# Optimization experiments

Hardware: AMD Instinct MI355X
Metric: run time of the kernel (lower is better)

The kernel has to match this reference:

```python
import jax, jax.numpy as jnp
import numpy as np

B, SQ, SKV, D = 4, 4096, 4096, 64

def setup_inputs() -> dict:
    key = jax.random.key(0)
    kq, kk, kv = jax.random.split(key, 3)
    return {
        "q": jax.random.normal(kq, (B, SQ, D), dtype=jnp.float32),
        "k": jax.random.normal(kk, (B, SKV, D), dtype=jnp.float32),
        "v": jax.random.normal(kv, (B, SKV, D), dtype=jnp.float32),
        "inv_scale_factor": 8,
        "is_training": 0,
    }

def reference(q, k, v, inv_scale_factor, is_training):
    # qk = q @ k^T, divided by inv_scale_factor, softmax over keys
    scores = jnp.einsum("bqd,bkd->bqk", q, k) / inv_scale_factor  # [B,SQ,SKV]
    attn = jax.nn.softmax(scores, axis=-1)
    # dropout is deterministic identity (eval mode, is_training=0)
    out = jnp.einsum("bqk,bkd->bqd", attn, v)  # [B,SQ,D]
    # should_apply_residual before loop
    out = out + q
    # 3-iteration chain: residual add + normalization add (+2q), dropout (identity),
    # sigmoid, clamp(0,1)
    for _ in range(3):
        out = out + 2.0 * q
        out = jax.nn.sigmoid(out)
        out = jnp.clip(out, 0.0, 1.0)
    return out
```

## Files before the change

### kernel.cpp

```cpp
#include <hip/hip_runtime.h>

#define SQd 4096
#define SKVd 4096
#define DDIM 64
#define BK 32
#define NG 8
#define NTILES (SKVd / BK)
#define TPG (NTILES / NG)
#define TILE_BYTES 2048
#define KWS_BYTES (4 * NTILES * TILE_BYTES)
#define BROWS 32

typedef float floatx4 __attribute__((ext_vector_type(4)));

__device__ inline long long mk64(int lo, int hi) {
    int2 t; t.x = lo; t.y = hi;
    return __builtin_bit_cast(long long, t);
}
template <bool HI>
__device__ inline int pk2(float a, float b, int old) {
    return __builtin_amdgcn_cvt_pk_fp8_f32(a, b, old, HI);
}

struct CombS {
    float Ored[BROWS][4][68];
    float Lred[BROWS][NG];
};

__global__ __launch_bounds__(256)
void prepack_kernel(const float* __restrict__ k, const float* __restrict__ v,
                    char* __restrict__ ws)
{
    __shared__ __align__(16) float Kt[BK][68];
    __shared__ __align__(16) float Vt[BK][68];

    const int blk  = blockIdx.x;
    const int b    = blk >> 7;
    const int tile = blk & (NTILES - 1);
    const int tid  = threadIdx.x;

    const size_t base = ((size_t)b * SKVd + tile * BK) * DDIM;
    {
        const int row = tid >> 3, col = (tid & 7) * 8;
        const float4 k0 = *(const float4*)(k + base + (size_t)row * DDIM + col);
        const float4 k1 = *(const float4*)(k + base + (size_t)row * DDIM + col + 4);
        *(float4*)&Kt[row][col] = k0; *(float4*)&Kt[row][col + 4] = k1;
        const float4 v0 = *(const float4*)(v + base + (size_t)row * DDIM + col);
        const float4 v1 = *(const float4*)(v + base + (size_t)row * DDIM + col + 4);
        *(float4*)&Vt[row][col] = v0; *(float4*)&Vt[row][col + 4] = v1;
    }
    __syncthreads();

    const int lane = tid & 63;
    const int l16  = lane & 15;
    const int quad = lane >> 4;
    const int f    = tid >> 6;

    int w[4];
    size_t off;
    if (f < 2) {
        const float* s0 = &Kt[f * 16 + l16][quad * 8];
        const float* s1 = &Kt[f * 16 + l16][32 + quad * 8];
        w[0] = pk2<false>(s0[0], s0[1], 0); w[0] = pk2<true>(s0[2], s0[3], w[0]);
        w[1] = pk2<false>(s0[4], s0[5], 0); w[1] = pk2<true>(s0[6], s0[7], w[1]);
        w[2] = pk2<false>(s1[0], s1[1], 0); w[2] = pk2<true>(s1[2], s1[3], w[2]);
        w[3] = pk2<false>(s1[4], s1[5], 0); w[3] = pk2<true>(s1[6], s1[7], w[3]);
        off = ((size_t)(b * NTILES + tile) * 2 + f) * 1024 + lane * 16;
    } else {
        const int p = f - 2;
        float vv[16];
        #pragma unroll
        for (int j2 = 0; j2 < 16; ++j2) {
            const int nb = 2 * p + (j2 >> 3);
            const int j  = j2 & 7;
            vv[j2] = Vt[16 * (j >> 2) + quad * 4 + (j & 3)][nb * 16 + l16];
        }
        #pragma unroll
        for (int i = 0; i < 4; ++i) {
            w[i] = pk2<false>(vv[4 * i], vv[4 * i + 1], 0);
            w[i] = pk2<true>(vv[4 * i + 2], vv[4 * i + 3], w[i]);
        }
        off = (size_t)KWS_BYTES + ((size_t)(b * NTILES + tile) * 2 + p) * 1024 + lane * 16;
    }
    int4 o4; o4.x = w[0]; o4.y = w[1]; o4.z = w[2]; o4.w = w[3];
    *(int4*)(ws + off) = o4;
}

__global__ __launch_bounds__(512, 4)
void fattn_kernel(const float* __restrict__ q, const int* __restrict__ isf_p,
                  const char* __restrict__ kws, const char* __restrict__ vws,
                  float* __restrict__ out)
{
    __shared__ __align__(16) CombS C;

    const int tid  = threadIdx.x;
    const int g    = tid >> 6;
    const int lane = tid & 63;
    const int l16  = lane & 15;
    const int quad = lane >> 4;

    const int bidx  = blockIdx.x;
    const int b     = bidx >> 7;
    const int qbase = (bidx & 127) * BROWS;

    const float scale = 1.44269504088896340736f / (float)(*isf_p);
    const float SINIT = -4.0f * 1.44269504088896340736f;

    long long qf[2][2];
    #pragma unroll
    for (int qg = 0; qg < 2; ++qg) {
        const int qrow = qbase + qg * 16 + l16;
        const float* qp = q + ((size_t)b * SQd + qrow) * DDIM + quad * 8;
        #pragma unroll
        for (int dh = 0; dh < 2; ++dh) {
            const float4 a0 = *(const float4*)(qp + dh * 32);
            const float4 a1 = *(const float4*)(qp + dh * 32 + 4);
            int lo = pk2<false>(a0.x * scale, a0.y * scale, 0);
            lo     = pk2<true>(a0.z * scale, a0.w * scale, lo);
            int hi = pk2<false>(a1.x * scale, a1.y * scale, 0);
            hi     = pk2<true>(a1.z * scale, a1.w * scale, hi);
            qf[qg][dh] = mk64(lo, hi);
        }
    }

    const char* kg = kws + (size_t)(b * NTILES + g * TPG) * TILE_BYTES + lane * 16;
    const char* vg = vws + (size_t)(b * NTILES + g * TPG) * TILE_BYTES + lane * 16;
    const int phase = bidx & (TPG - 1);

    floatx4 o[2][4];
    float l_acc[2];
    #pragma unroll
    for (int qg = 0; qg < 2; ++qg) {
        l_acc[qg] = 0.0f;
        #pragma unroll
        for (int nb = 0; nb < 4; ++nb)
            #pragma unroll
            for (int r = 0; r < 4; ++r) o[qg][nb][r] = 0.0f;
    }
    const floatx4 sinit = {SINIT, SINIT, SINIT, SINIT};

    auto load = [&](int4* kd, int4* vd, int t) {
        const size_t off = (size_t)((t + phase) & (TPG - 1)) * TILE_BYTES;
        kd[0] = *(const int4*)(kg + off);
        kd[1] = *(const int4*)(kg + off + 1024);
        vd[0] = *(const int4*)(vg + off);
        vd[1] = *(const int4*)(vg + off + 1024);
    };
    auto compute = [&](const int4* kc, const int4* vc) {
        const long long k00 = mk64(kc[0].x, kc[0].y), k01 = mk64(kc[0].z, kc[0].w);
        const long long k10 = mk64(kc[1].x, kc[1].y), k11 = mk64(kc[1].z, kc[1].w);
        const long long v0 = mk64(vc[0].x, vc[0].y), v1 = mk64(vc[0].z, vc[0].w);
        const long long v2 = mk64(vc[1].x, vc[1].y), v3 = mk64(vc[1].z, vc[1].w);
        #pragma unroll
        for (int qg = 0; qg < 2; ++qg) {
            floatx4 s0 = sinit, s1 = sinit;
            s0 = __builtin_amdgcn_mfma_f32_16x16x32_fp8_fp8(k00, qf[qg][0], s0, 0, 0, 0);
            s0 = __builtin_amdgcn_mfma_f32_16x16x32_fp8_fp8(k01, qf[qg][1], s0, 0, 0, 0);
            s1 = __builtin_amdgcn_mfma_f32_16x16x32_fp8_fp8(k10, qf[qg][0], s1, 0, 0, 0);
            s1 = __builtin_amdgcn_mfma_f32_16x16x32_fp8_fp8(k11, qf[qg][1], s1, 0, 0, 0);
            const float p00 = __builtin_amdgcn_exp2f(s0[0]);
            const float p01 = __builtin_amdgcn_exp2f(s0[1]);
            const float p02 = __builtin_amdgcn_exp2f(s0[2]);
            const float p03 = __builtin_amdgcn_exp2f(s0[3]);
            const float p10 = __builtin_amdgcn_exp2f(s1[0]);
            const float p11 = __builtin_amdgcn_exp2f(s1[1]);
            const float p12 = __builtin_amdgcn_exp2f(s1[2]);
            const float p13 = __builtin_amdgcn_exp2f(s1[3]);
            l_acc[qg] += (p00 + p01) + (p02 + p03) + (p10 + p11) + (p12 + p13);
            int lo = pk2<false>(p00, p01, 0); lo = pk2<true>(p02, p03, lo);
            int hi = pk2<false>(p10, p11, 0); hi = pk2<true>(p12, p13, hi);
            const long long pf = mk64(lo, hi);
            o[qg][0] = __builtin_amdgcn_mfma_f32_16x16x32_fp8_fp8(pf, v0, o[qg][0], 0, 0, 0);
            o[qg][1] = __builtin_amdgcn_mfma_f32_16x16x32_fp8_fp8(pf, v1, o[qg][1], 0, 0, 0);
            o[qg][2] = __builtin_amdgcn_mfma_f32_16x16x32_fp8_fp8(pf, v2, o[qg][2], 0, 0, 0);
            o[qg][3] = __builtin_amdgcn_mfma_f32_16x16x32_fp8_fp8(pf, v3, o[qg][3], 0, 0, 0);
        }
    };

    int4 kb0[2], vb0[2], kb1[2], vb1[2];
    load(kb0, vb0, 0);
    #pragma unroll
    for (int t = 0; t < TPG / 2; ++t) {
        load(kb1, vb1, 2 * t + 1);
        compute(kb0, vb0);
        load(kb0, vb0, (2 * t + 2) & (TPG - 1));
        compute(kb1, vb1);
    }

    #pragma unroll
    for (int qg = 0; qg < 2; ++qg) {
        l_acc[qg] += __shfl_xor(l_acc[qg], 16);
        l_acc[qg] += __shfl_xor(l_acc[qg], 32);
    }
    if (quad == 0) {
        #pragma unroll
        for (int qg = 0; qg < 2; ++qg)
            C.Lred[qg * 16 + l16][g] = l_acc[qg];
    }

    if (g < 4) {
        #pragma unroll
        for (int qg = 0; qg < 2; ++qg)
            #pragma unroll
            for (int nb = 0; nb < 4; ++nb)
                #pragma unroll
                for (int r = 0; r < 4; ++r)
                    C.Ored[qg * 16 + quad * 4 + r][g][nb * 16 + l16] = o[qg][nb][r];
    }
    __syncthreads();
    if (g >= 4) {
        #pragma unroll
        for (int qg = 0; qg < 2; ++qg)
            #pragma unroll
            for (int nb = 0; nb < 4; ++nb)
                #pragma unroll
                for (int r = 0; r < 4; ++r)
                    C.Ored[qg * 16 + quad * 4 + r][g - 4][nb * 16 + l16] += o[qg][nb][r];
    }
    __syncthreads();

    {
        const int row = tid >> 4;
        const int d4  = (tid & 15) * 4;
        float l = 0.0f;
        #pragma unroll
        for (int gg = 0; gg < NG; ++gg) l += C.Lred[row][gg];
        const float rl = 1.0f / l;
        float xs[4] = {0.f, 0.f, 0.f, 0.f};
        #pragma unroll
        for (int s = 0; s < 4; ++s) {
            const float4 t4 = *(const float4*)&C.Ored[row][s][d4];
            xs[0] += t4.x; xs[1] += t4.y; xs[2] += t4.z; xs[3] += t4.w;
        }
        const size_t idx = ((size_t)b * SQd + qbase + row) * DDIM + d4;
        const float4 q4 = *(const float4*)(q + idx);
        const float qs[4] = {q4.x, q4.y, q4.z, q4.w};
        #pragma unroll
        for (int c = 0; c < 4; ++c) {
            float x = xs[c] * rl + qs[c];
            #pragma unroll
            for (int itc = 0; itc < 3; ++itc) {
                x = x + 2.0f * qs[c];
                x = 1.0f / (1.0f + __expf(-x));
                x = fminf(fmaxf(x, 0.0f), 1.0f);
            }
            xs[c] = x;
        }
        const float4 r4 = {xs[0], xs[1], xs[2], xs[3]};
        *(float4*)(out + idx) = r4;
    }
}

extern "C" void kernel_launch(void* const* d_in, const int* in_sizes, int n_in,
                              void* d_out, int out_size, void* d_ws, size_t ws_size,
                              hipStream_t stream) {
    const float* q = (const float*)d_in[0];
    const float* k = (const float*)d_in[1];
    const float* v = (const float*)d_in[2];
    const int* isf = (const int*)d_in[3];
    float* out = (float*)d_out;
    char* ws = (char*)d_ws;

    prepack_kernel<<<dim3(4 * NTILES), dim3(256), 0, stream>>>(k, v, ws);

    const int nblocks = 4 * (SQd / BROWS);
    fattn_kernel<<<dim3(nblocks), dim3(512), 0, stream>>>(
        q, isf, ws, ws + KWS_BYTES, out);
}
```

Measured before the change: 88.14 us.

## Switch attention MFMAs to 32x32x64 scaled FP8 with repacked K/V layout

Replaces the 16x16x32 FP8 MFMA sequence with the gfx950 32x32x64 scaled f8f6f4 MFMA for both QK^T and PV, processing 64-key chunks per iteration. The prepack kernel writes K and V in a new fragment layout to match the larger MFMA operands, and the loop now loads the next chunk's K and V separately, each after the MFMAs that consume the current one. This is meant to cut MFMA instruction count and issue overhead and to give fewer, wider loads. In exchange it raises per-thread register pressure (16-wide accumulators and score vectors) and depends on the new layout being correct.

```diff
diff --git a/kernel.cpp b/kernel.cpp
--- a/kernel.cpp
+++ b/kernel.cpp
@@ -6,20 +6,26 @@
 #define BK 32
 #define NG 8
 #define NTILES (SKVd / BK)
+#define NCHUNK (NTILES / 2)
 #define TPG (NTILES / NG)
-#define TILE_BYTES 2048
-#define KWS_BYTES (4 * NTILES * TILE_BYTES)
+#define CPG (TPG / 2)
+#define KWS_BYTES ((size_t)4 * NTILES * 2048)
 #define BROWS 32
 
-typedef float floatx4 __attribute__((ext_vector_type(4)));
-
-__device__ inline long long mk64(int lo, int hi) {
-    int2 t; t.x = lo; t.y = hi;
-    return __builtin_bit_cast(long long, t);
-}
+typedef float floatx4  __attribute__((ext_vector_type(4)));
+typedef float floatx16 __attribute__((ext_vector_type(16)));
+typedef int   intx8    __attribute__((ext_vector_type(8)));
+
 template <bool HI>
 __device__ inline int pk2(float a, float b, int old) {
     return __builtin_amdgcn_cvt_pk_fp8_f32(a, b, old, HI);
+}
+
+__device__ inline intx8 mk8(int4 a, int4 b) {
+    intx8 r;
+    r[0] = a.x; r[1] = a.y; r[2] = a.z; r[3] = a.w;
+    r[4] = b.x; r[5] = b.y; r[6] = b.z; r[7] = b.w;
+    return r;
 }
 
 struct CombS {
@@ -52,38 +58,35 @@
     __syncthreads();
 
     const int lane = tid & 63;
-    const int l16  = lane & 15;
-    const int quad = lane >> 4;
-    const int f    = tid >> 6;
-
-    int w[4];
-    size_t off;
-    if (f < 2) {
-        const float* s0 = &Kt[f * 16 + l16][quad * 8];
-        const float* s1 = &Kt[f * 16 + l16][32 + quad * 8];
-        w[0] = pk2<false>(s0[0], s0[1], 0); w[0] = pk2<true>(s0[2], s0[3], w[0]);
-        w[1] = pk2<false>(s0[4], s0[5], 0); w[1] = pk2<true>(s0[6], s0[7], w[1]);
-        w[2] = pk2<false>(s1[0], s1[1], 0); w[2] = pk2<true>(s1[2], s1[3], w[2]);
-        w[3] = pk2<false>(s1[4], s1[5], 0); w[3] = pk2<true>(s1[6], s1[7], w[3]);
-        off = ((size_t)(b * NTILES + tile) * 2 + f) * 1024 + lane * 16;
-    } else {
-        const int p = f - 2;
-        float vv[16];
-        #pragma unroll
-        for (int j2 = 0; j2 < 16; ++j2) {
-            const int nb = 2 * p + (j2 >> 3);
-            const int j  = j2 & 7;
-            vv[j2] = Vt[16 * (j >> 2) + quad * 4 + (j & 3)][nb * 16 + l16];
-        }
-        #pragma unroll
-        for (int i = 0; i < 4; ++i) {
-            w[i] = pk2<false>(vv[4 * i], vv[4 * i + 1], 0);
-            w[i] = pk2<true>(vv[4 * i + 2], vv[4 * i + 3], w[i]);
-        }
-        off = (size_t)KWS_BYTES + ((size_t)(b * NTILES + tile) * 2 + p) * 1024 + lane * 16;
-    }
-    int4 o4; o4.x = w[0]; o4.y = w[1]; o4.z = w[2]; o4.w = w[3];
-    *(int4*)(ws + off) = o4;
+    const int q4   = tid >> 6;
+    const int l31  = lane & 31;
+    const int u    = lane >> 5;
+
+    {
+        const float* s = &Kt[l31][u * 32 + q4 * 8];
+        int w0 = pk2<false>(s[0], s[1], 0); w0 = pk2<true>(s[2], s[3], w0);
+        int w1 = pk2<false>(s[4], s[5], 0); w1 = pk2<true>(s[6], s[7], w1);
+        int2 o2; o2.x = w0; o2.y = w1;
+        *(int2*)(ws + (size_t)(b * NTILES + tile) * 2048 + lane * 32 + q4 * 8) = o2;
+    }
+    {
+        const int h  = q4 >> 1;
+        const int rh = (q4 & 1) * 8;
+        float p[8];
+        #pragma unroll
+        for (int i = 0; i < 8; ++i) {
+            const int r   = rh + i;
+            const int key = (r & 3) + 8 * (r >> 2) + 4 * u;
+            p[i] = Vt[key][h * 32 + l31];
+        }
+        int w0 = pk2<false>(p[0], p[1], 0); w0 = pk2<true>(p[2], p[3], w0);
+        int w1 = pk2<false>(p[4], p[5], 0); w1 = pk2<true>(p[6], p[7], w1);
+        int2 o2; o2.x = w0; o2.y = w1;
+        const size_t voff = KWS_BYTES
+            + ((size_t)(b * NCHUNK + (tile >> 1)) * 2 + h) * 2048
+            + lane * 32 + (tile & 1) * 16 + rh;
+        *(int2*)(ws + voff) = o2;
+    }
 }
 
 __global__ __launch_bounds__(512, 4)
@@ -91,13 +94,13 @@
                   const char* __restrict__ kws, const char* __restrict__ vws,
                   float* __restrict__ out)
 {
-    __shared__ __align__(16) CombS C;
+    __shared__ CombS C;
 
     const int tid  = threadIdx.x;
     const int g    = tid >> 6;
     const int lane = tid & 63;
-    const int l16  = lane & 15;
-    const int quad = lane >> 4;
+    const int l31  = lane & 31;
+    const int u    = lane >> 5;
 
     const int bidx  = blockIdx.x;
     const int b     = bidx >> 7;
@@ -106,116 +109,97 @@
     const float scale = 1.44269504088896340736f / (float)(*isf_p);
     const float SINIT = -4.0f * 1.44269504088896340736f;
 
-    long long qf[2][2];
+    intx8 qf;
+    {
+        const float* qp = q + ((size_t)b * SQd + qbase + l31) * DDIM + u * 32;
+        #pragma unroll
+        for (int d = 0; d < 8; ++d) {
+            const float4 a = *(const float4*)(qp + 4 * d);
+            int w = pk2<false>(a.x * scale, a.y * scale, 0);
+            w     = pk2<true >(a.z * scale, a.w * scale, w);
+            qf[d] = w;
+        }
+    }
+
+    const char* kg = kws + (size_t)(b * NTILES + g * TPG) * 2048 + lane * 32;
+    const char* vg = vws + (size_t)(b * NCHUNK + g * CPG) * 4096 + lane * 32;
+    const int cph  = bidx & (CPG - 1);
+
+    floatx16 sinit16, o0, o1;
     #pragma unroll
-    for (int qg = 0; qg < 2; ++qg) {
-        const int qrow = qbase + qg * 16 + l16;
-        const float* qp = q + ((size_t)b * SQd + qrow) * DDIM + quad * 8;
-        #pragma unroll
-        for (int dh = 0; dh < 2; ++dh) {
-            const float4 a0 = *(const float4*)(qp + dh * 32);
-            const float4 a1 = *(const float4*)(qp + dh * 32 + 4);
-            int lo = pk2<false>(a0.x * scale, a0.y * scale, 0);
-            lo     = pk2<true>(a0.z * scale, a0.w * scale, lo);
-            int hi = pk2<false>(a1.x * scale, a1.y * scale, 0);
-            hi     = pk2<true>(a1.z * scale, a1.w * scale, hi);
-            qf[qg][dh] = mk64(lo, hi);
-        }
-    }
-
-    const char* kg = kws + (size_t)(b * NTILES + g * TPG) * TILE_BYTES + lane * 16;
-    const char* vg = vws + (size_t)(b * NTILES + g * TPG) * TILE_BYTES + lane * 16;
-    const int phase = bidx & (TPG - 1);
-
-    floatx4 o[2][4];
-    float l_acc[2];
+    for (int i = 0; i < 16; ++i) { sinit16[i] = SINIT; o0[i] = 0.f; o1[i] = 0.f; }
+    float l_acc = 0.f;
+
+    int4 kA0, kA1, kB0, kB1, vA0, vA1, vB0, vB1;
+    auto loadK = [&](int c) {
+        const size_t off = (size_t)((c + cph) & (CPG - 1)) * 4096;
+        kA0 = *(const int4*)(kg + off);        kA1 = *(const int4*)(kg + off + 16);
+        kB0 = *(const int4*)(kg + off + 2048); kB1 = *(const int4*)(kg + off + 2064);
+    };
+    auto loadV = [&](int c) {
+        const size_t off = (size_t)((c + cph) & (CPG - 1)) * 4096;
+        vA0 = *(const int4*)(vg + off);        vA1 = *(const int4*)(vg + off + 16);
+        vB0 = *(const int4*)(vg + off + 2048); vB1 = *(const int4*)(vg + off + 2064);
+    };
+
+    loadK(0); loadV(0);
     #pragma unroll
-    for (int qg = 0; qg < 2; ++qg) {
-        l_acc[qg] = 0.0f;
-        #pragma unroll
-        for (int nb = 0; nb < 4; ++nb)
-            #pragma unroll
-            for (int r = 0; r < 4; ++r) o[qg][nb][r] = 0.0f;
-    }
-    const floatx4 sinit = {SINIT, SINIT, SINIT, SINIT};
-
-    auto load = [&](int4* kd, int4* vd, int t) {
-        const size_t off = (size_t)((t + phase) & (TPG - 1)) * TILE_BYTES;
-        kd[0] = *(const int4*)(kg + off);
-        kd[1] = *(const int4*)(kg + off + 1024);
-        vd[0] = *(const int4*)(vg + off);
-        vd[1] = *(const int4*)(vg + off + 1024);
-    };
-    auto compute = [&](const int4* kc, const int4* vc) {
-        const long long k00 = mk64(kc[0].x, kc[0].y), k01 = mk64(kc[0].z, kc[0].w);
-        const long long k10 = mk64(kc[1].x, kc[1].y), k11 = mk64(kc[1].z, kc[1].w);
-        const long long v0 = mk64(vc[0].x, vc[0].y), v1 = mk64(vc[0].z, vc[0].w);
-        const long long v2 = mk64(vc[1].x, vc[1].y), v3 = mk64(vc[1].z, vc[1].w);
-        #pragma unroll
-        for (int qg = 0; qg < 2; ++qg) {
-            floatx4 s0 = sinit, s1 = sinit;
-            s0 = __builtin_amdgcn_mfma_f32_16x16x32_fp8_fp8(k00, qf[qg][0], s0, 0, 0, 0);
-            s0 = __builtin_amdgcn_mfma_f32_16x16x32_fp8_fp8(k01, qf[qg][1], s0, 0, 0, 0);
-            s1 = __builtin_amdgcn_mfma_f32_16x16x32_fp8_fp8(k10, qf[qg][0], s1, 0, 0, 0);
-            s1 = __builtin_amdgcn_mfma_f32_16x16x32_fp8_fp8(k11, qf[qg][1], s1, 0, 0, 0);
-            const float p00 = __builtin_amdgcn_exp2f(s0[0]);
-            const float p01 = __builtin_amdgcn_exp2f(s0[1]);
-            const float p02 = __builtin_amdgcn_exp2f(s0[2]);
-            const float p03 = __builtin_amdgcn_exp2f(s0[3]);
-            const float p10 = __builtin_amdgcn_exp2f(s1[0]);
-            const float p11 = __builtin_amdgcn_exp2f(s1[1]);
-            const float p12 = __builtin_amdgcn_exp2f(s1[2]);
-            const float p13 = __builtin_amdgcn_exp2f(s1[3]);
-            l_acc[qg] += (p00 + p01) + (p02 + p03) + (p10 + p11) + (p12 + p13);
-            int lo = pk2<false>(p00, p01, 0); lo = pk2<true>(p02, p03, lo);
-            int hi = pk2<false>(p10, p11, 0); hi = pk2<true>(p12, p13, hi);
-            const long long pf = mk64(lo, hi);
-            o[qg][0] = __builtin_amdgcn_mfma_f32_16x16x32_fp8_fp8(pf, v0, o[qg][0], 0, 0, 0);
-            o[qg][1] = __builtin_amdgcn_mfma_f32_16x16x32_fp8_fp8(pf, v1, o[qg][1], 0, 0, 0);
-            o[qg][2] = __builtin_amdgcn_mfma_f32_16x16x32_fp8_fp8(pf, v2, o[qg][2], 0, 0, 0);
-            o[qg][3] = __builtin_amdgcn_mfma_f32_16x16x32_fp8_fp8(pf, v3, o[qg][3], 0, 0, 0);
-        }
-    };
-
-    int4 kb0[2], vb0[2], kb1[2], vb1[2];
-    load(kb0, vb0, 0);
-    #pragma unroll
-    for (int t = 0; t < TPG / 2; ++t) {
-        load(kb1, vb1, 2 * t + 1);
-        compute(kb0, vb0);
-        load(kb0, vb0, (2 * t + 2) & (TPG - 1));
-        compute(kb1, vb1);
-    }
-
-    #pragma unroll
-    for (int qg = 0; qg < 2; ++qg) {
-        l_acc[qg] += __shfl_xor(l_acc[qg], 16);
-        l_acc[qg] += __shfl_xor(l_acc[qg], 32);
-    }
-    if (quad == 0) {
-        #pragma unroll
-        for (int qg = 0; qg < 2; ++qg)
-            C.Lred[qg * 16 + l16][g] = l_acc[qg];
-    }
+    for (int c = 0; c < CPG; ++c) {
+        floatx16 se = __builtin_amdgcn_mfma_scale_f32_32x32x64_f8f6f4(
+            mk8(kA0, kA1), qf, sinit16, 0, 0, 0, 0x7F7F7F7F, 0, 0x7F7F7F7F);
+        floatx16 so = __builtin_amdgcn_mfma_scale_f32_32x32x64_f8f6f4(
+            mk8(kB0, kB1), qf, sinit16, 0, 0, 0, 0x7F7F7F7F, 0, 0x7F7F7F7F);
+        if (c + 1 < CPG) loadK(c + 1);
+
+        float pe[16], po[16];
+        #pragma unroll
+        for (int r = 0; r < 16; ++r) pe[r] = __builtin_amdgcn_exp2f(se[r]);
+        #pragma unroll
+        for (int r = 0; r < 16; ++r) po[r] = __builtin_amdgcn_exp2f(so[r]);
+
+        l_acc += ((((pe[0] + pe[1]) + (pe[2] + pe[3])) + ((pe[4] + pe[5]) + (pe[6] + pe[7])))
+               + (((pe[8] + pe[9]) + (pe[10] + pe[11])) + ((pe[12] + pe[13]) + (pe[14] + pe[15]))));
+        l_acc += ((((po[0] + po[1]) + (po[2] + po[3])) + ((po[4] + po[5]) + (po[6] + po[7])))
+               + (((po[8] + po[9]) + (po[10] + po[11])) + ((po[12] + po[13]) + (po[14] + po[15]))));
+
+        intx8 pa;
+        #pragma unroll
+        for (int d2 = 0; d2 < 4; ++d2) {
+            int w = pk2<false>(pe[4 * d2], pe[4 * d2 + 1], 0);
+            pa[d2] = pk2<true>(pe[4 * d2 + 2], pe[4 * d2 + 3], w);
+        }
+        #pragma unroll
+        for (int d2 = 0; d2 < 4; ++d2) {
+            int w = pk2<false>(po[4 * d2], po[4 * d2 + 1], 0);
+            pa[4 + d2] = pk2<true>(po[4 * d2 + 2], po[4 * d2 + 3], w);
+        }
+
+        o0 = __builtin_amdgcn_mfma_scale_f32_32x32x64_f8f6f4(
+            pa, mk8(vA0, vA1), o0, 0, 0, 0, 0x7F7F7F7F, 0, 0x7F7F7F7F);
+        o1 = __builtin_amdgcn_mfma_scale_f32_32x32x64_f8f6f4(
+            pa, mk8(vB0, vB1), o1, 0, 0, 0, 0x7F7F7F7F, 0, 0x7F7F7F7F);
+        if (c + 1 < CPG) loadV(c + 1);
+    }
+
+    l_acc += __shfl_xor(l_acc, 32);
+    if (u == 0) C.Lred[l31][g] = l_acc;
 
     if (g < 4) {
         #pragma unroll
-        for (int qg = 0; qg < 2; ++qg)
-            #pragma unroll
-            for (int nb = 0; nb < 4; ++nb)
-                #pragma unroll
-                for (int r = 0; r < 4; ++r)
-                    C.Ored[qg * 16 + quad * 4 + r][g][nb * 16 + l16] = o[qg][nb][r];
+        for (int r = 0; r < 16; ++r) {
+            const int row = (r & 3) + 8 * (r >> 2) + 4 * u;
+            C.Ored[row][g][l31]      = o0[r];
+            C.Ored[row][g][32 + l31] = o1[r];
+        }
     }
     __syncthreads();
     if (g >= 4) {
         #pragma unroll
-        for (int qg = 0; qg < 2; ++qg)
-            #pragma unroll
-            for (int nb = 0; nb < 4; ++nb)
-                #pragma unroll
-                for (int r = 0; r < 4; ++r)
-                    C.Ored[qg * 16 + quad * 4 + r][g - 4][nb * 16 + l16] += o[qg][nb][r];
+        for (int r = 0; r < 16; ++r) {
+            const int row = (r & 3) + 8 * (r >> 2) + 4 * u;
+            C.Ored[row][g - 4][l31]      += o0[r];
+            C.Ored[row][g - 4][32 + l31] += o1[r];
+        }
     }
     __syncthreads();
 
@@ -233,8 +217,8 @@
             xs[0] += t4.x; xs[1] += t4.y; xs[2] += t4.z; xs[3] += t4.w;
         }
         const size_t idx = ((size_t)b * SQd + qbase + row) * DDIM + d4;
-        const float4 q4 = *(const float4*)(q + idx);
-        const float qs[4] = {q4.x, q4.y, q4.z, q4.w};
+        const float4 q4v = *(const float4*)(q + idx);
+        const float qs[4] = {q4v.x, q4v.y, q4v.z, q4v.w};
         #pragma unroll
         for (int c = 0; c < 4; ++c) {
             float x = xs[c] * rl + qs[c];
```

Measured after the change: 120.6 us. 1.37x slower.

## Halve query rows per block to 16 and drop manual K/V double-buffering

Applied to the files above, without the earlier changes.

Each block now handles 16 query rows instead of 32, doubling the grid and halving per-wave accumulator registers, with launch bounds raised to request 8 blocks per CU. The manually unrolled, software-pipelined K/V load loop is replaced by a simple non-unrolled loop that loads and computes each tile in turn. The aim is higher occupancy so that wave switching hides load latency. In exchange, each loaded K/V tile is reused by only one 16-row query group, so K/V workspace traffic per query doubles and the explicit prefetch overlap is lost.

```diff
diff --git a/kernel.cpp b/kernel.cpp
--- a/kernel.cpp
+++ b/kernel.cpp
@@ -8,8 +8,8 @@
 #define NTILES (SKVd / BK)
 #define TPG (NTILES / NG)
 #define TILE_BYTES 2048
-#define KWS_BYTES (4 * NTILES * TILE_BYTES)
-#define BROWS 32
+#define KWS_BYTES ((size_t)4 * NTILES * TILE_BYTES)
+#define BROWS 16
 
 typedef float floatx4 __attribute__((ext_vector_type(4)));
 
@@ -86,12 +86,12 @@
     *(int4*)(ws + off) = o4;
 }
 
-__global__ __launch_bounds__(512, 4)
+__global__ __launch_bounds__(512, 8)
 void fattn_kernel(const float* __restrict__ q, const int* __restrict__ isf_p,
                   const char* __restrict__ kws, const char* __restrict__ vws,
                   float* __restrict__ out)
 {
-    __shared__ __align__(16) CombS C;
+    __shared__ CombS C;
 
     const int tid  = threadIdx.x;
     const int g    = tid >> 6;
@@ -100,143 +100,119 @@
     const int quad = lane >> 4;
 
     const int bidx  = blockIdx.x;
-    const int b     = bidx >> 7;
-    const int qbase = (bidx & 127) * BROWS;
+    const int b     = bidx >> 8;
+    const int qbase = (bidx & 255) * BROWS;
 
     const float scale = 1.44269504088896340736f / (float)(*isf_p);
     const float SINIT = -4.0f * 1.44269504088896340736f;
 
-    long long qf[2][2];
-    #pragma unroll
-    for (int qg = 0; qg < 2; ++qg) {
-        const int qrow = qbase + qg * 16 + l16;
-        const float* qp = q + ((size_t)b * SQd + qrow) * DDIM + quad * 8;
-        #pragma unroll
-        for (int dh = 0; dh < 2; ++dh) {
-            const float4 a0 = *(const float4*)(qp + dh * 32);
-            const float4 a1 = *(const float4*)(qp + dh * 32 + 4);
-            int lo = pk2<false>(a0.x * scale, a0.y * scale, 0);
-            lo     = pk2<true>(a0.z * scale, a0.w * scale, lo);
-            int hi = pk2<false>(a1.x * scale, a1.y * scale, 0);
-            hi     = pk2<true>(a1.z * scale, a1.w * scale, hi);
-            qf[qg][dh] = mk64(lo, hi);
-        }
+    long long qf0, qf1;
+    {
+        const float* qp = q + ((size_t)b * SQd + qbase + l16) * DDIM + quad * 8;
+        const float4 a0 = *(const float4*)(qp);
+        const float4 a1 = *(const float4*)(qp + 4);
+        int lo = pk2<false>(a0.x * scale, a0.y * scale, 0);
+        lo     = pk2<true>(a0.z * scale, a0.w * scale, lo);
+        int hi = pk2<false>(a1.x * scale, a1.y * scale, 0);
+        hi     = pk2<true>(a1.z * scale, a1.w * scale, hi);
+        qf0 = mk64(lo, hi);
+        const float4 b0 = *(const float4*)(qp + 32);
+        const float4 b1 = *(const float4*)(qp + 36);
+        lo = pk2<false>(b0.x * scale, b0.y * scale, 0);
+        lo = pk2<true>(b0.z * scale, b0.w * scale, lo);
+        hi = pk2<false>(b1.x * scale, b1.y * scale, 0);
+        hi = pk2<true>(b1.z * scale, b1.w * scale, hi);
+        qf1 = mk64(lo, hi);
     }
 
     const char* kg = kws + (size_t)(b * NTILES + g * TPG) * TILE_BYTES + lane * 16;
     const char* vg = vws + (size_t)(b * NTILES + g * TPG) * TILE_BYTES + lane * 16;
     const int phase = bidx & (TPG - 1);
 
-    floatx4 o[2][4];
-    float l_acc[2];
+    floatx4 o[4];
+    float l_acc = 0.0f;
     #pragma unroll
-    for (int qg = 0; qg < 2; ++qg) {
-        l_acc[qg] = 0.0f;
+    for (int nb = 0; nb < 4; ++nb)
+        #pragma unroll
+        for (int r = 0; r < 4; ++r) o[nb][r] = 0.0f;
+    const floatx4 sinit = {SINIT, SINIT, SINIT, SINIT};
+
+    #pragma unroll 1
+    for (int t = 0; t < TPG; ++t) {
+        const size_t off = (size_t)((t + phase) & (TPG - 1)) * TILE_BYTES;
+        const int4 kc0 = *(const int4*)(kg + off);
+        const int4 kc1 = *(const int4*)(kg + off + 1024);
+        const int4 vc0 = *(const int4*)(vg + off);
+        const int4 vc1 = *(const int4*)(vg + off + 1024);
+
+        const long long k00 = mk64(kc0.x, kc0.y), k01 = mk64(kc0.z, kc0.w);
+        const long long k10 = mk64(kc1.x, kc1.y), k11 = mk64(kc1.z, kc1.w);
+        const long long v0 = mk64(vc0.x, vc0.y), v1 = mk64(vc0.z, vc0.w);
+        const long long v2 = mk64(vc1.x, vc1.y), v3 = mk64(vc1.z, vc1.w);
+
+        floatx4 s0 = sinit, s1 = sinit;
+        s0 = __builtin_amdgcn_mfma_f32_16x16x32_fp8_fp8(k00, qf0, s0, 0, 0, 0);
+        s0 = __builtin_amdgcn_mfma_f32_16x16x32_fp8_fp8(k01, qf1, s0, 0, 0, 0);
+        s1 = __builtin_amdgcn_mfma_f32_16x16x32_fp8_fp8(k10, qf0, s1, 0, 0, 0);
+        s1 = __builtin_amdgcn_mfma_f32_16x16x32_fp8_fp8(k11, qf1, s1, 0, 0, 0);
+
+        const float p00 = __builtin_amdgcn_exp2f(s0[0]);
+        const float p01 = __builtin_amdgcn_exp2f(s0[1]);
+        const float p02 = __builtin_amdgcn_exp2f(s0[2]);
+        const float p03 = __builtin_amdgcn_exp2f(s0[3]);
+        const float p10 = __builtin_amdgcn_exp2f(s1[0]);
+        const float p11 = __builtin_amdgcn_exp2f(s1[1]);
+        const float p12 = __builtin_amdgcn_exp2f(s1[2]);
+        const float p13 = __builtin_amdgcn_exp2f(s1[3]);
+        l_acc += (p00 + p01) + (p02 + p03) + (p10 + p11) + (p12 + p13);
+        int lo = pk2<false>(p00, p01, 0); lo = pk2<true>(p02, p03, lo);
+        int hi = pk2<false>(p10, p11, 0); hi = pk2<true>(p12, p13, hi);
+        const long long pf = mk64(lo, hi);
+        o[0] = __builtin_amdgcn_mfma_f32_16x16x32_fp8_fp8(pf, v0, o[0], 0, 0, 0);
+        o[1] = __builtin_amdgcn_mfma_f32_16x16x32_fp8_fp8(pf, v1, o[1], 0, 0, 0);
+        o[2] = __builtin_amdgcn_mfma_f32_16x16x32_fp8_fp8(pf, v2, o[2], 0, 0, 0);
+        o[3] = __builtin_amdgcn_mfma_f32_16x16x32_fp8_fp8(pf, v3, o[3], 0, 0, 0);
+    }
+
+    l_acc += __shfl_xor(l_acc, 16);
+    l_acc += __shfl_xor(l_acc, 32);
+    if (quad == 0) C.Lred[l16][g] = l_acc;
+
+    if (g < 4) {
         #pragma unroll
         for (int nb = 0; nb < 4; ++nb)
             #pragma unroll
-            for (int r = 0; r < 4; ++r) o[qg][nb][r] = 0.0f;
-    }
-    const floatx4 sinit = {SINIT, SINIT, SINIT, SINIT};
-
-    auto load = [&](int4* kd, int4* vd, int t) {
-        const size_t off = (size_t)((t + phase) & (TPG - 1)) * TILE_BYTES;
-        kd[0] = *(const int4*)(kg + off);
-        kd[1] = *(const int4*)(kg + off + 1024);
-        vd[0] = *(const int4*)(vg + off);
-        vd[1] = *(const int4*)(vg + off + 1024);
-    };
-    auto compute = [&](const int4* kc, const int4* vc) {
-        const long long k00 = mk64(kc[0].x, kc[0].y), k01 = mk64(kc[0].z, kc[0].w);
-        const long long k10 = mk64(kc[1].x, kc[1].y), k11 = mk64(kc[1].z, kc[1].w);
-        const long long v0 = mk64(vc[0].x, vc[0].y), v1 = mk64(vc[0].z, vc[0].w);
-        const long long v2 = mk64(vc[1].x, vc[1].y), v3 = mk64(vc[1].z, vc[1].w);
-        #pragma unroll
-        for (int qg = 0; qg < 2; ++qg) {
-            floatx4 s0 = sinit, s1 = sinit;
-            s0 = __builtin_amdgcn_mfma_f32_16x16x32_fp8_fp8(k00, qf[qg][0], s0, 0, 0, 0);
-            s0 = __builtin_amdgcn_mfma_f32_16x16x32_fp8_fp8(k01, qf[qg][1], s0, 0, 0, 0);
-            s1 = __builtin_amdgcn_mfma_f32_16x16x32_fp8_fp8(k10, qf[qg][0], s1, 0, 0, 0);
-            s1 = __builtin_amdgcn_mfma_f32_16x16x32_fp8_fp8(k11, qf[qg][1], s1, 0, 0, 0);
-            const float p00 = __builtin_amdgcn_exp2f(s0[0]);
-            const float p01 = __builtin_amdgcn_exp2f(s0[1]);
-            const float p02 = __builtin_amdgcn_exp2f(s0[2]);
-            const float p03 = __builtin_amdgcn_exp2f(s0[3]);
-            const float p10 = __builtin_amdgcn_exp2f(s1[0]);
-            const float p11 = __builtin_amdgcn_exp2f(s1[1]);
-            const float p12 = __builtin_amdgcn_exp2f(s1[2]);
-            const float p13 = __builtin_amdgcn_exp2f(s1[3]);
-            l_acc[qg] += (p00 + p01) + (p02 + p03) + (p10 + p11) + (p12 + p13);
-            int lo = pk2<false>(p00, p01, 0); lo = pk2<true>(p02, p03, lo);
-            int hi = pk2<false>(p10, p11, 0); hi = pk2<true>(p12, p13, hi);
-            const long long pf = mk64(lo, hi);
-            o[qg][0] = __builtin_amdgcn_mfma_f32_16x16x32_fp8_fp8(pf, v0, o[qg][0], 0, 0, 0);
-            o[qg][1] = __builtin_amdgcn_mfma_f32_16x16x32_fp8_fp8(pf, v1, o[qg][1], 0, 0, 0);
-            o[qg][2] = __builtin_amdgcn_mfma_f32_16x16x32_fp8_fp8(pf, v2, o[qg][2], 0, 0, 0);
-            o[qg][3] = __builtin_amdgcn_mfma_f32_16x16x32_fp8_fp8(pf, v3, o[qg][3], 0, 0, 0);
-        }
-    };
-
-    int4 kb0[2], vb0[2], kb1[2], vb1[2];
-    load(kb0, vb0, 0);
-    #pragma unroll
-    for (int t = 0; t < TPG / 2; ++t) {
-        load(kb1, vb1, 2 * t + 1);
-        compute(kb0, vb0);
-        load(kb0, vb0, (2 * t + 2) & (TPG - 1));
-        compute(kb1, vb1);
-    }
-
-    #pragma unroll
-    for (int qg = 0; qg < 2; ++qg) {
-        l_acc[qg] += __shfl_xor(l_acc[qg], 16);
-        l_acc[qg] += __shfl_xor(l_acc[qg], 32);
-    }
-    if (quad == 0) {
-        #pragma unroll
-        for (int qg = 0; qg < 2; ++qg)
-            C.Lred[qg * 16 + l16][g] = l_acc[qg];
-    }
-
-    if (g < 4) {
-        #pragma unroll
-        for (int qg = 0; qg < 2; ++qg)
-            #pragma unroll
-            for (int nb = 0; nb < 4; ++nb)
-                #pragma unroll
-                for (int r = 0; r < 4; ++r)
-                    C.Ored[qg * 16 + quad * 4 + r][g][nb * 16 + l16] = o[qg][nb][r];
+            for (int r = 0; r < 4; ++r)
+                C.Ored[quad * 4 + r][g][nb * 16 + l16] = o[nb][r];
     }
     __syncthreads();
     if (g >= 4) {
         #pragma unroll
-        for (int qg = 0; qg < 2; ++qg)
+        for (int nb = 0; nb < 4; ++nb)
             #pragma unroll
-            for (int nb = 0; nb < 4; ++nb)
-                #pragma unroll
-                for (int r = 0; r < 4; ++r)
-                    C.Ored[qg * 16 + quad * 4 + r][g - 4][nb * 16 + l16] += o[qg][nb][r];
+            for (int r = 0; r < 4; ++r)
+                C.Ored[quad * 4 + r][g - 4][nb * 16 + l16] += o[nb][r];
     }
     __syncthreads();
 
     {
-        const int row = tid >> 4;
-        const int d4  = (tid & 15) * 4;
+        const int row = tid >> 5;
+        const int d2  = (tid & 31) * 2;
         float l = 0.0f;
         #pragma unroll
         for (int gg = 0; gg < NG; ++gg) l += C.Lred[row][gg];
         const float rl = 1.0f / l;
-        float xs[4] = {0.f, 0.f, 0.f, 0.f};
+        float xs[2] = {0.f, 0.f};
         #pragma unroll
         for (int s = 0; s < 4; ++s) {
-            const float4 t4 = *(const float4*)&C.Ored[row][s][d4];
-            xs[0] += t4.x; xs[1] += t4.y; xs[2] += t4.z; xs[3] += t4.w;
-        }
-        const size_t idx = ((size_t)b * SQd + qbase + row) * DDIM + d4;
-        const float4 q4 = *(const float4*)(q + idx);
-        const float qs[4] = {q4.x, q4.y, q4.z, q4.w};
-        #pragma unroll
-        for (int c = 0; c < 4; ++c) {
+            xs[0] += C.Ored[row][s][d2];
+            xs[1] += C.Ored[row][s][d2 + 1];
+        }
+        const size_t idx = ((size_t)b * SQd + qbase + row) * DDIM + d2;
+        const float2 q2 = *(const float2*)(q + idx);
+        const float qs[2] = {q2.x, q2.y};
+        #pragma unroll
+        for (int c = 0; c < 2; ++c) {
             float x = xs[c] * rl + qs[c];
             #pragma unroll
             for (int itc = 0; itc < 3; ++itc) {
@@ -246,8 +222,8 @@
             }
             xs[c] = x;
         }
-        const float4 r4 = {xs[0], xs[1], xs[2], xs[3]};
-        *(float4*)(out + idx) = r4;
+        const float2 r2 = {xs[0], xs[1]};
+        *(float2*)(out + idx) = r2;
     }
 }
 
```

Result: slower. 95.51 us (+8.4%).
